# Performance work log

Hardware: AMD Instinct MI355X
Metric: run time of the kernel (lower is better)

The kernel has to match this reference:

```python
import jax, jax.numpy as jnp
import numpy as np

BETA_MIN = 0.1
BETA_MAX = 20.0

def _marginals(t):
    # VP-SDE closed forms: mean(t) = exp(-0.25 t^2 (bmax-bmin) - 0.5 t bmin), std = sqrt(1 - mean^2)
    log_mean = -0.25 * t ** 2 * (BETA_MAX - BETA_MIN) - 0.5 * t * BETA_MIN
    mean = jnp.exp(log_mean)
    std = jnp.sqrt(jnp.maximum(1.0 - jnp.exp(2.0 * log_mean), 1e-12))
    return mean, std

def setup_inputs() -> dict:
    key = jax.random.key(0)
    k1, k2, k3 = jax.random.split(key, 3)
    N, M, D = 4096, 16384, 128
    x = jax.random.normal(k1, (N, D), dtype=jnp.float32)
    t = jax.random.uniform(k2, (N,), dtype=jnp.float32, minval=0.05, maxval=1.0)
    train_data = jax.random.normal(k3, (M, D), dtype=jnp.float32)
    return {"x": x, "t": t, "train_data": train_data}

def reference(x, t, train_data):
    # x: (N, D), t: (N,), train_data: (M, D)
    mean, sigma = _marginals(t)                       # (N,), (N,)
    inv_var = 1.0 / (sigma ** 2)                      # (N,)
    # logpdf[n, i] = -0.5 * ||x_n - mean_n * y_i||^2 / sigma_n^2
    # expanded: ||x_n||^2 - 2 mean_n <x_n, y_i> + mean_n^2 ||y_i||^2
    xy = jnp.einsum('nd,md->nm', x, train_data)       # (N, M) GEMM
    x2 = jnp.sum(x ** 2, axis=1)                      # (N,)
    y2 = jnp.sum(train_data ** 2, axis=1)             # (M,)
    sq = x2[:, None] - 2.0 * mean[:, None] * xy + (mean ** 2)[:, None] * y2[None, :]
    logpdf = -0.5 * sq * inv_var[:, None]             # (N, M)
    weights = jax.nn.softmax(logpdf, axis=1)          # (N, M)
    evals = weights @ train_data                      # (N, D)
    evals = jnp.where(jnp.isnan(evals), 0.0, evals)
    return (evals - x) * inv_var[:, None]
```

## Files before the change

### kernel.cpp

```cpp
#include <hip/hip_runtime.h>

typedef unsigned int u32;
typedef unsigned short u16;
typedef short s16x8 __attribute__((ext_vector_type(8)));
typedef float f32x4 __attribute__((ext_vector_type(4)));

#define BETA_MIN 0.1f
#define BETA_MAX 20.0f

#define MFMA16(a, b, c) __builtin_amdgcn_mfma_f32_16x16x32_bf16(a, b, c, 0, 0, 0)

__device__ __forceinline__ u16 f2bf(float f) {
    u32 u = __float_as_uint(f);
    u32 r = u + 0x7FFFu + ((u >> 16) & 1u);
    return (u16)(r >> 16);
}
__device__ __forceinline__ float bf2f(u16 h) {
    return __uint_as_float(((u32)h) << 16);
}
__device__ __forceinline__ f32x4 zero4() {
    f32x4 z = {0.f, 0.f, 0.f, 0.f};
    return z;
}

template <int CTRL>
__device__ __forceinline__ float dppf(float x) {
    return __int_as_float(__builtin_amdgcn_update_dpp(
        0, __float_as_int(x), CTRL, 0xF, 0xF, false));
}
__device__ __forceinline__ float rowmax16(float x) {
    x = fmaxf(x, dppf<0xB1>(x));
    x = fmaxf(x, dppf<0x4E>(x));
    x = fmaxf(x, dppf<0x124>(x));
    x = fmaxf(x, dppf<0x128>(x));
    return x;
}
__device__ __forceinline__ float rowsum16(float x) {
    x += dppf<0xB1>(x);
    x += dppf<0x4E>(x);
    x += dppf<0x124>(x);
    x += dppf<0x128>(x);
    return x;
}


__global__ void rows_kernel(const float* __restrict__ t, float* __restrict__ rowc, int N) {
    int n = blockIdx.x * blockDim.x + threadIdx.x;
    if (n >= N) return;
    float tv   = t[n];
    float lm   = -0.25f * tv * tv * (BETA_MAX - BETA_MIN) - 0.5f * tv * BETA_MIN;
    float mean = __expf(lm);
    float e2   = __expf(2.0f * lm);
    float s2   = fmaxf(1.0f - e2, 1e-12f);
    float iv   = 1.0f / s2;
    rowc[n * 4 + 0] = mean * iv;
    rowc[n * 4 + 1] = -0.5f * mean * mean * iv;
    rowc[n * 4 + 2] = iv;
    rowc[n * 4 + 3] = 0.f;
}

__global__ void conv_hilo(const float* __restrict__ src, u16* __restrict__ hi,
                          u16* __restrict__ lo, int total4) {
    int idx = blockIdx.x * blockDim.x + threadIdx.x;
    if (idx >= total4) return;
    float4 v = ((const float4*)src)[idx];
    float f[4] = {v.x, v.y, v.z, v.w};
    u32 hp[2], lp[2];
    u16 h[4], l[4];
#pragma unroll
    for (int j = 0; j < 4; ++j) {
        h[j] = f2bf(f[j]);
        l[j] = f2bf(f[j] - bf2f(h[j]));
    }
    hp[0] = (u32)h[0] | ((u32)h[1] << 16);
    hp[1] = (u32)h[2] | ((u32)h[3] << 16);
    lp[0] = (u32)l[0] | ((u32)l[1] << 16);
    lp[1] = (u32)l[2] | ((u32)l[3] << 16);
    ((uint2*)hi)[idx] = make_uint2(hp[0], hp[1]);
    ((uint2*)lo)[idx] = make_uint2(lp[0], lp[1]);
}

__global__ void vt_y2_kernel(const float* __restrict__ train, u16* __restrict__ Vt,
                             float* __restrict__ y2, int M) {
    int wave = threadIdx.x >> 6, lane = threadIdx.x & 63;
    int m = blockIdx.x * 4 + wave;
    const float* row = train + (size_t)m * 128;
    float2 v = *(const float2*)(row + lane * 2);
    u16 h0 = f2bf(v.x), h1 = f2bf(v.y);
    Vt[(size_t)(lane * 2 + 0) * M + m] = h0;
    Vt[(size_t)(lane * 2 + 1) * M + m] = h1;
    float s = v.x * v.x + v.y * v.y;
#pragma unroll
    for (int d = 1; d < 64; d <<= 1) s += __shfl_xor(s, d);
    if (lane == 0) y2[m] = s;
}

__global__ __launch_bounds__(256, 4)
void flash_kernel(const u16* __restrict__ Khi, const u16* __restrict__ Klo,
                  const u16* __restrict__ Vt,  const u16* __restrict__ Qhi,
                  const u16* __restrict__ Qlo, const float* __restrict__ rowc,
                  const float* __restrict__ y2, float* __restrict__ partO,
                  float* __restrict__ partML, int N, int M, int mchunk) {
    __shared__ u16 sKhi[32][136];
    __shared__ u16 sKlo[32][136];
    __shared__ u16 sVt[128][40];
    __shared__ u16 sP[4][16][40];

    const int tid  = threadIdx.x;
    const int wave = tid >> 6, lane = tid & 63;
    const int l15  = lane & 15, quad = lane >> 4;
    const int qb = blockIdx.x, chunk = blockIdx.y;
    const int q0 = qb * 64 + wave * 16;
    const int m_begin = chunk * mchunk;

    s16x8 qh[4], ql[4];
    {
        int row = q0 + l15;
        const u16* ph = Qhi + (size_t)row * 128;
        const u16* pl = Qlo + (size_t)row * 128;
#pragma unroll
        for (int kb = 0; kb < 4; ++kb) {
            qh[kb] = *(const s16x8*)(ph + kb * 32 + quad * 8);
            ql[kb] = *(const s16x8*)(pl + kb * 32 + quad * 8);
        }
    }
    float av[4], bv[4];
#pragma unroll
    for (int k = 0; k < 4; ++k) {
        int r = q0 + quad * 4 + k;
        av[k] = rowc[r * 4 + 0];
        bv[k] = rowc[r * 4 + 1];
    }

    f32x4 O[8];
#pragma unroll
    for (int db = 0; db < 8; ++db) O[db] = zero4();
    float m_run[4], l_run[4];
#pragma unroll
    for (int k = 0; k < 4; ++k) { m_run[k] = -INFINITY; l_run[k] = 0.f; }

    for (int mt = 0; mt < mchunk; mt += 32) {
        const int m0 = m_begin + mt;
        __syncthreads();
#pragma unroll
        for (int r = 0; r < 2; ++r) {
            int c = tid + r * 256;
            int row = c >> 4, col = (c & 15) * 8;
            *(uint4*)&sKhi[row][col] = *(const uint4*)(Khi + (size_t)(m0 + row) * 128 + col);
            *(uint4*)&sKlo[row][col] = *(const uint4*)(Klo + (size_t)(m0 + row) * 128 + col);
            int dd = c >> 2, mc = (c & 3) * 8;
            *(uint4*)&sVt[dd][mc] = *(const uint4*)(Vt + (size_t)dd * M + m0 + mc);
        }
        __syncthreads();

        float y2v0 = y2[m0 + l15];
        float y2v1 = y2[m0 + 16 + l15];

        f32x4 S[2];
        S[0] = zero4(); S[1] = zero4();
#pragma unroll
        for (int kb = 0; kb < 4; ++kb) {
            s16x8 bh0 = *(const s16x8*)&sKhi[l15][kb * 32 + quad * 8];
            s16x8 bh1 = *(const s16x8*)&sKhi[16 + l15][kb * 32 + quad * 8];
            s16x8 bl0 = *(const s16x8*)&sKlo[l15][kb * 32 + quad * 8];
            s16x8 bl1 = *(const s16x8*)&sKlo[16 + l15][kb * 32 + quad * 8];
            S[0] = MFMA16(qh[kb], bh0, S[0]);
            S[0] = MFMA16(ql[kb], bh0, S[0]);
            S[0] = MFMA16(qh[kb], bl0, S[0]);
            S[1] = MFMA16(qh[kb], bh1, S[1]);
            S[1] = MFMA16(ql[kb], bh1, S[1]);
            S[1] = MFMA16(qh[kb], bl1, S[1]);
        }

#pragma unroll
        for (int k = 0; k < 4; ++k) {
            float s0 = av[k] * S[0][k] + bv[k] * y2v0;
            float s1 = av[k] * S[1][k] + bv[k] * y2v1;
            float rm    = rowmax16(fmaxf(s0, s1));
            float mnew  = fmaxf(m_run[k], rm);
            float alpha = __expf(m_run[k] - mnew);
            float p0 = __expf(s0 - mnew);
            float p1 = __expf(s1 - mnew);
            m_run[k] = mnew;
            l_run[k] = l_run[k] * alpha + (p0 + p1);
            sP[wave][quad * 4 + k][l15]      = f2bf(p0);
            sP[wave][quad * 4 + k][16 + l15] = f2bf(p1);
#pragma unroll
            for (int db = 0; db < 8; ++db) O[db][k] *= alpha;
        }
        asm volatile("s_waitcnt lgkmcnt(0)" ::: "memory");

        s16x8 pa = *(const s16x8*)&sP[wave][l15][quad * 8];
#pragma unroll
        for (int db = 0; db < 8; ++db) {
            s16x8 vb = *(const s16x8*)&sVt[db * 16 + l15][quad * 8];
            O[db] = MFMA16(pa, vb, O[db]);
        }
    }

#pragma unroll
    for (int db = 0; db < 8; ++db) {
#pragma unroll
        for (int k = 0; k < 4; ++k) {
            int row = q0 + quad * 4 + k;
            partO[((size_t)chunk * N + row) * 128 + db * 16 + l15] = O[db][k];
        }
    }
#pragma unroll
    for (int k = 0; k < 4; ++k) {
        float lsum = rowsum16(l_run[k]);
        if (l15 == 0) {
            int row = q0 + quad * 4 + k;
            partML[((size_t)chunk * N + row) * 2 + 0] = m_run[k];
            partML[((size_t)chunk * N + row) * 2 + 1] = lsum;
        }
    }
}

__global__ void combine_kernel(const float* __restrict__ partO, const float* __restrict__ partML,
                               const float* __restrict__ x, const float* __restrict__ rowc,
                               float* __restrict__ out, int N, int split) {
    int n = blockIdx.x, d = threadIdx.x;
    float Mx = -INFINITY;
    for (int c = 0; c < split; ++c)
        Mx = fmaxf(Mx, partML[((size_t)c * N + n) * 2]);
    float L = 0.f, acc = 0.f;
    for (int c = 0; c < split; ++c) {
        float w = __expf(partML[((size_t)c * N + n) * 2] - Mx);
        L   += w * partML[((size_t)c * N + n) * 2 + 1];
        acc += w * partO[((size_t)c * N + n) * 128 + d];
    }
    float evals = acc / L;
    if (evals != evals) evals = 0.f;
    float iv = rowc[n * 4 + 2];
    out[(size_t)n * 128 + d] = (evals - x[(size_t)n * 128 + d]) * iv;
}

extern "C" void kernel_launch(void* const* d_in, const int* in_sizes, int n_in,
                              void* d_out, int out_size, void* d_ws, size_t ws_size,
                              hipStream_t stream) {
    const float* x     = (const float*)d_in[0];
    const float* t     = (const float*)d_in[1];
    const float* train = (const float*)d_in[2];
    float* out = (float*)d_out;

    const int N = in_sizes[1];
    const int D = 128;
    const int M = in_sizes[2] / D;

    char* ws = (char*)d_ws;
    size_t off = 0;
    auto alloc = [&](size_t bytes) -> void* {
        void* p = ws + off;
        off = (off + bytes + 255) & ~(size_t)255;
        return p;
    };
    u16* Khi   = (u16*)alloc((size_t)M * D * 2);
    u16* Klo   = (u16*)alloc((size_t)M * D * 2);
    u16* Vt    = (u16*)alloc((size_t)M * D * 2);
    u16* Qhi   = (u16*)alloc((size_t)N * D * 2);
    u16* Qlo   = (u16*)alloc((size_t)N * D * 2);
    float* rowc = (float*)alloc((size_t)N * 16);
    float* y2   = (float*)alloc((size_t)M * 4);
    size_t base = off;
    size_t per  = (size_t)N * D * 4 + (size_t)N * 8 + 512;
    int split = 16;
    while (split > 1 && base + per * split > ws_size) split >>= 1;
    float* partO  = (float*)alloc((size_t)split * N * D * 4);
    float* partML = (float*)alloc((size_t)split * N * 8);

    rows_kernel<<<(N + 255) / 256, 256, 0, stream>>>(t, rowc, N);
    conv_hilo<<<(N * D / 4 + 255) / 256, 256, 0, stream>>>(x, Qhi, Qlo, N * D / 4);
    conv_hilo<<<(M * D / 4 + 255) / 256, 256, 0, stream>>>(train, Khi, Klo, M * D / 4);
    vt_y2_kernel<<<M / 4, 256, 0, stream>>>(train, Vt, y2, M);

    int mchunk = M / split;
    dim3 grid(N / 64, split);
    flash_kernel<<<grid, 256, 0, stream>>>(Khi, Klo, Vt, Qhi, Qlo, rowc, y2,
                                           partO, partML, N, M, mchunk);
    combine_kernel<<<N, 128, 0, stream>>>(partO, partML, x, rowc, out, N, split);
}
```

Before: 212.4 us.

## Prefetch K/V tiles into registers, lazily rescale softmax, transpose V via LDS

```diff
diff --git a/kernel.cpp b/kernel.cpp
--- a/kernel.cpp
+++ b/kernel.cpp
@@ -21,6 +21,11 @@
 __device__ __forceinline__ f32x4 zero4() {
     f32x4 z = {0.f, 0.f, 0.f, 0.f};
     return z;
+}
+__device__ __forceinline__ u32 cvtpk_bf16(float a, float b) {
+    u32 r;
+    asm("v_cvt_pk_bf16_f32 %0, %1, %2" : "=v"(r) : "v"(a), "v"(b));
+    return r;
 }
 
 template <int CTRL>
@@ -80,19 +85,39 @@
     ((uint2*)lo)[idx] = make_uint2(lp[0], lp[1]);
 }
 
-__global__ void vt_y2_kernel(const float* __restrict__ train, u16* __restrict__ Vt,
-                             float* __restrict__ y2, int M) {
-    int wave = threadIdx.x >> 6, lane = threadIdx.x & 63;
-    int m = blockIdx.x * 4 + wave;
-    const float* row = train + (size_t)m * 128;
-    float2 v = *(const float2*)(row + lane * 2);
-    u16 h0 = f2bf(v.x), h1 = f2bf(v.y);
-    Vt[(size_t)(lane * 2 + 0) * M + m] = h0;
-    Vt[(size_t)(lane * 2 + 1) * M + m] = h1;
-    float s = v.x * v.x + v.y * v.y;
-#pragma unroll
-    for (int d = 1; d < 64; d <<= 1) s += __shfl_xor(s, d);
-    if (lane == 0) y2[m] = s;
+__global__ __launch_bounds__(256)
+void vt_y2_kernel(const float* __restrict__ train, u16* __restrict__ Vt,
+                  float* __restrict__ y2, int M) {
+    __shared__ u16 T[128][66];
+    const int t = threadIdx.x;
+    const int m0 = blockIdx.x * 64;
+    const int g = t >> 5, ln = t & 31;
+#pragma unroll
+    for (int i = 0; i < 8; ++i) {
+        int lr = i * 8 + g;
+        const float* row = train + (size_t)(m0 + lr) * 128;
+        float acc = 0.f;
+#pragma unroll
+        for (int j = 0; j < 4; ++j) {
+            float v = row[ln + 32 * j];
+            T[ln + 32 * j][lr] = f2bf(v);
+            acc += v * v;
+        }
+#pragma unroll
+        for (int d = 16; d >= 1; d >>= 1) acc += __shfl_xor(acc, d, 32);
+        if (ln == 0) y2[m0 + lr] = acc;
+    }
+    __syncthreads();
+#pragma unroll
+    for (int i = 0; i < 4; ++i) {
+        int c = i * 256 + t;
+        int d = c >> 3, mo = (c & 7) * 8;
+        u32 w0 = *(const u32*)&T[d][mo + 0];
+        u32 w1 = *(const u32*)&T[d][mo + 2];
+        u32 w2 = *(const u32*)&T[d][mo + 4];
+        u32 w3 = *(const u32*)&T[d][mo + 6];
+        *(uint4*)(Vt + (size_t)d * M + m0 + mo) = make_uint4(w0, w1, w2, w3);
+    }
 }
 
 __global__ __launch_bounds__(256, 4)
@@ -139,54 +164,86 @@
 #pragma unroll
     for (int k = 0; k < 4; ++k) { m_run[k] = -INFINITY; l_run[k] = 0.f; }
 
+    const int srow = tid >> 4, scol = (tid & 15) * 8;
+    const int sdd  = tid >> 2, smc  = (tid & 3) * 8;
+    const u16* gKh = Khi + (size_t)(m_begin + srow) * 128 + scol;
+    const u16* gKl = Klo + (size_t)(m_begin + srow) * 128 + scol;
+    const u16* gVt = Vt  + (size_t)sdd * M + m_begin + smc;
+    const float* gy2 = y2 + m_begin + l15;
+
+    uint4 Lh0 = *(const uint4*)gKh, Lh1 = *(const uint4*)(gKh + 16 * 128);
+    uint4 Ll0 = *(const uint4*)gKl, Ll1 = *(const uint4*)(gKl + 16 * 128);
+    uint4 Lv0 = *(const uint4*)gVt, Lv1 = *(const uint4*)(gVt + (size_t)64 * M);
+    float y2c0 = gy2[0], y2c1 = gy2[16];
+    float y2n0 = 0.f, y2n1 = 0.f;
+
     for (int mt = 0; mt < mchunk; mt += 32) {
-        const int m0 = m_begin + mt;
         __syncthreads();
-#pragma unroll
-        for (int r = 0; r < 2; ++r) {
-            int c = tid + r * 256;
-            int row = c >> 4, col = (c & 15) * 8;
-            *(uint4*)&sKhi[row][col] = *(const uint4*)(Khi + (size_t)(m0 + row) * 128 + col);
-            *(uint4*)&sKlo[row][col] = *(const uint4*)(Klo + (size_t)(m0 + row) * 128 + col);
-            int dd = c >> 2, mc = (c & 3) * 8;
-            *(uint4*)&sVt[dd][mc] = *(const uint4*)(Vt + (size_t)dd * M + m0 + mc);
-        }
+        *(uint4*)&sKhi[srow][scol]      = Lh0;
+        *(uint4*)&sKhi[srow + 16][scol] = Lh1;
+        *(uint4*)&sKlo[srow][scol]      = Ll0;
+        *(uint4*)&sKlo[srow + 16][scol] = Ll1;
+        *(uint4*)&sVt[sdd][smc]         = Lv0;
+        *(uint4*)&sVt[sdd + 64][smc]    = Lv1;
         __syncthreads();
 
-        float y2v0 = y2[m0 + l15];
-        float y2v1 = y2[m0 + 16 + l15];
-
-        f32x4 S[2];
-        S[0] = zero4(); S[1] = zero4();
+        gKh += 32 * 128; gKl += 32 * 128; gVt += 32; gy2 += 32;
+        if (mt + 32 < mchunk) {
+            Lh0 = *(const uint4*)gKh; Lh1 = *(const uint4*)(gKh + 16 * 128);
+            Ll0 = *(const uint4*)gKl; Ll1 = *(const uint4*)(gKl + 16 * 128);
+            Lv0 = *(const uint4*)gVt; Lv1 = *(const uint4*)(gVt + (size_t)64 * M);
+            y2n0 = gy2[0]; y2n1 = gy2[16];
+        }
+
+        f32x4 S0 = zero4(), S1 = zero4();
 #pragma unroll
         for (int kb = 0; kb < 4; ++kb) {
             s16x8 bh0 = *(const s16x8*)&sKhi[l15][kb * 32 + quad * 8];
             s16x8 bh1 = *(const s16x8*)&sKhi[16 + l15][kb * 32 + quad * 8];
             s16x8 bl0 = *(const s16x8*)&sKlo[l15][kb * 32 + quad * 8];
             s16x8 bl1 = *(const s16x8*)&sKlo[16 + l15][kb * 32 + quad * 8];
-            S[0] = MFMA16(qh[kb], bh0, S[0]);
-            S[0] = MFMA16(ql[kb], bh0, S[0]);
-            S[0] = MFMA16(qh[kb], bl0, S[0]);
-            S[1] = MFMA16(qh[kb], bh1, S[1]);
-            S[1] = MFMA16(ql[kb], bh1, S[1]);
-            S[1] = MFMA16(qh[kb], bl1, S[1]);
-        }
-
+            S0 = MFMA16(qh[kb], bh0, S0);
+            S0 = MFMA16(ql[kb], bh0, S0);
+            S0 = MFMA16(qh[kb], bl0, S0);
+            S1 = MFMA16(qh[kb], bh1, S1);
+            S1 = MFMA16(ql[kb], bh1, S1);
+            S1 = MFMA16(qh[kb], bl1, S1);
+        }
+
+        float s0[4], s1[4];
+        int need = 0;
 #pragma unroll
         for (int k = 0; k < 4; ++k) {
-            float s0 = av[k] * S[0][k] + bv[k] * y2v0;
-            float s1 = av[k] * S[1][k] + bv[k] * y2v1;
-            float rm    = rowmax16(fmaxf(s0, s1));
-            float mnew  = fmaxf(m_run[k], rm);
-            float alpha = __expf(m_run[k] - mnew);
-            float p0 = __expf(s0 - mnew);
-            float p1 = __expf(s1 - mnew);
-            m_run[k] = mnew;
-            l_run[k] = l_run[k] * alpha + (p0 + p1);
-            sP[wave][quad * 4 + k][l15]      = f2bf(p0);
-            sP[wave][quad * 4 + k][16 + l15] = f2bf(p1);
-#pragma unroll
-            for (int db = 0; db < 8; ++db) O[db][k] *= alpha;
+            s0[k] = fmaf(av[k], S0[k], bv[k] * y2c0);
+            s1[k] = fmaf(av[k], S1[k], bv[k] * y2c1);
+            need |= (fmaxf(s0[k], s1[k]) > m_run[k] + 8.0f) ? 1 : 0;
+        }
+        if (__any(need)) {
+#pragma unroll
+            for (int k = 0; k < 4; ++k) {
+                float rm    = rowmax16(fmaxf(s0[k], s1[k]));
+                float mnew  = fmaxf(m_run[k], rm);
+                float alpha = __expf(m_run[k] - mnew);
+                float p0 = __expf(s0[k] - mnew);
+                float p1 = __expf(s1[k] - mnew);
+                m_run[k] = mnew;
+                l_run[k] = l_run[k] * alpha + (p0 + p1);
+                u32 pk = cvtpk_bf16(p0, p1);
+                sP[wave][quad * 4 + k][l15]      = (u16)pk;
+                sP[wave][quad * 4 + k][16 + l15] = (u16)(pk >> 16);
+#pragma unroll
+                for (int db = 0; db < 8; ++db) O[db][k] *= alpha;
+            }
+        } else {
+#pragma unroll
+            for (int k = 0; k < 4; ++k) {
+                float p0 = __expf(s0[k] - m_run[k]);
+                float p1 = __expf(s1[k] - m_run[k]);
+                l_run[k] += p0 + p1;
+                u32 pk = cvtpk_bf16(p0, p1);
+                sP[wave][quad * 4 + k][l15]      = (u16)pk;
+                sP[wave][quad * 4 + k][16 + l15] = (u16)(pk >> 16);
+            }
         }
         asm volatile("s_waitcnt lgkmcnt(0)" ::: "memory");
 
@@ -196,6 +253,7 @@
             s16x8 vb = *(const s16x8*)&sVt[db * 16 + l15][quad * 8];
             O[db] = MFMA16(pa, vb, O[db]);
         }
+        y2c0 = y2n0; y2c1 = y2n1;
     }
 
 #pragma unroll
@@ -272,7 +330,7 @@
     rows_kernel<<<(N + 255) / 256, 256, 0, stream>>>(t, rowc, N);
     conv_hilo<<<(N * D / 4 + 255) / 256, 256, 0, stream>>>(x, Qhi, Qlo, N * D / 4);
     conv_hilo<<<(M * D / 4 + 255) / 256, 256, 0, stream>>>(train, Khi, Klo, M * D / 4);
-    vt_y2_kernel<<<M / 4, 256, 0, stream>>>(train, Vt, y2, M);
+    vt_y2_kernel<<<M / 64, 256, 0, stream>>>(train, Vt, y2, M);
 
     int mchunk = M / split;
     dim3 grid(N / 64, split);
```

Result: slower. 470.3 us (+121.4%).
